# Performance work log

Measured on AMD Instinct MI355X. Metric: run time of the kernel, lower is better.

Reference implementation:

```python
import jax, jax.numpy as jnp
import numpy as np

B, L, D, H = 2, 1024, 1024, 16
HD = D // H
HIDDEN = 4 * D
EPS = 1e-6
SCALE = HD ** -0.5

# RoPE tables (head_dim is even, so rope_dim == head_dim)
_inv_freq = 1.0 / (10000.0 ** (np.arange(0, HD, 2, dtype=np.float32) / HD))
_freqs = np.arange(L, dtype=np.float32)[:, None] * _inv_freq[None, :]          # [L, HD/2]
COS = jnp.asarray(np.concatenate([np.cos(_freqs), np.cos(_freqs)], -1))        # [L, HD]
SIN = jnp.asarray(np.concatenate([np.sin(_freqs), np.sin(_freqs)], -1))
MASK = jnp.tril(jnp.ones((L, L), dtype=bool))                                   # causal


def _clin(xr, xi, Wr, Wi, br=None, bi=None):
    # complex linear: (a+bi)(c+di), weights stored [out, in] as in torch
    r = xr @ Wr.T - xi @ Wi.T
    i = xr @ Wi.T + xi @ Wr.T
    if br is not None:
        r = r + br
        i = i + bi
    return r, i


def _cln(xr, xi, gr, gi, br, bi):
    mr = xr.mean(-1, keepdims=True)
    mi = xi.mean(-1, keepdims=True)
    cr = xr - mr
    ci = xi - mi
    var = (cr * cr + ci * ci).mean(-1, keepdims=True)
    s = jnp.sqrt(var + EPS)
    nr = cr / s
    ni = ci / s
    return nr * gr - ni * gi + br, nr * gi + ni * gr + bi


def _rot_half(x):
    h = x.shape[-1] // 2
    return jnp.concatenate([-x[..., h:], x[..., :h]], -1)


def _rope(xr, xi):
    # apply same real rotation to real and imag parts (matches torch code)
    return (xr * COS + _rot_half(xr) * SIN, xi * COS + _rot_half(xi) * SIN)


def _split_heads(x):
    return x.reshape(B, L, H, HD).transpose(0, 2, 1, 3)  # [B,H,L,HD]


def _merge_heads(x):
    return x.transpose(0, 2, 1, 3).reshape(B, L, D)


def setup_inputs() -> dict:
    key = jax.random.key(0)
    ks = jax.random.split(key, 20)
    n = lambda k, shape, s=1.0: jax.random.normal(k, shape, dtype=jnp.float32) * s
    s_attn = (2.0 * (D + D)) ** -0.5
    s_fc1 = (2.0 * (D + HIDDEN)) ** -0.5
    s_fc2 = (2.0 * (HIDDEN + D)) ** -0.5
    return {
        'x_real': n(ks[0], (B, L, D)),
        'x_imag': n(ks[1], (B, L, D)),
        'Wq_r': n(ks[2], (D, D), s_attn), 'Wq_i': n(ks[3], (D, D), s_attn),
        'Wk_r': n(ks[4], (D, D), s_attn), 'Wk_i': n(ks[5], (D, D), s_attn),
        'Wv_r': n(ks[6], (D, D), s_attn), 'Wv_i': n(ks[7], (D, D), s_attn),
        'Wo_r': n(ks[8], (D, D), s_attn), 'Wo_i': n(ks[9], (D, D), s_attn),
        'bo_r': jnp.zeros((D,), jnp.float32), 'bo_i': jnp.zeros((D,), jnp.float32),
        'ln1_gr': jnp.ones((D,), jnp.float32), 'ln1_gi': jnp.zeros((D,), jnp.float32),
        'ln1_br': jnp.zeros((D,), jnp.float32), 'ln1_bi': jnp.zeros((D,), jnp.float32),
        'ln2_gr': jnp.ones((D,), jnp.float32), 'ln2_gi': jnp.zeros((D,), jnp.float32),
        'ln2_br': jnp.zeros((D,), jnp.float32), 'ln2_bi': jnp.zeros((D,), jnp.float32),
        'W1_r': n(ks[10], (HIDDEN, D), s_fc1), 'W1_i': n(ks[11], (HIDDEN, D), s_fc1),
        'b1_r': jnp.zeros((HIDDEN,), jnp.float32), 'b1_i': jnp.zeros((HIDDEN,), jnp.float32),
        'W2_r': n(ks[12], (D, HIDDEN), s_fc2), 'W2_i': n(ks[13], (D, HIDDEN), s_fc2),
        'b2_r': jnp.zeros((D,), jnp.float32), 'b2_i': jnp.zeros((D,), jnp.float32),
        'mod_b': n(ks[14], (HIDDEN,), 0.1),
    }


def reference(x_real, x_imag,
              Wq_r, Wq_i, Wk_r, Wk_i, Wv_r, Wv_i, Wo_r, Wo_i, bo_r, bo_i,
              ln1_gr, ln1_gi, ln1_br, ln1_bi, ln2_gr, ln2_gi, ln2_br, ln2_bi,
              W1_r, W1_i, b1_r, b1_i, W2_r, W2_i, b2_r, b2_i, mod_b):
    # --- attention sublayer (pre-LN) ---
    hr, hi = _cln(x_real, x_imag, ln1_gr, ln1_gi, ln1_br, ln1_bi)
    Qr, Qi = _clin(hr, hi, Wq_r, Wq_i)
    Kr, Ki = _clin(hr, hi, Wk_r, Wk_i)
    Vr, Vi = _clin(hr, hi, Wv_r, Wv_i)
    Qr, Qi, Kr, Ki = map(_split_heads, (Qr, Qi, Kr, Ki))
    Vr, Vi = _split_heads(Vr), _split_heads(Vi)
    Qr, Qi = _rope(Qr, Qi)
    Kr, Ki = _rope(Kr, Ki)
    # Hermitian inner product real part: Re(Q K*) = Qr.Kr + Qi.Ki
    scores = (jnp.einsum('bhld,bhmd->bhlm', Qr, Kr)
              + jnp.einsum('bhld,bhmd->bhlm', Qi, Ki)) * SCALE
    scores = jnp.where(MASK, scores, -jnp.inf)
    attn = jax.nn.softmax(scores, axis=-1)
    out_r = _merge_heads(jnp.einsum('bhlm,bhmd->bhld', attn, Vr))
    out_i = _merge_heads(jnp.einsum('bhlm,bhmd->bhld', attn, Vi))
    out_r, out_i = _clin(out_r, out_i, Wo_r, Wo_i, bo_r, bo_i)
    ar = x_real + out_r
    ai = x_imag + out_i
    # --- feed-forward sublayer (pre-LN) ---
    hr, hi = _cln(ar, ai, ln2_gr, ln2_gi, ln2_br, ln2_bi)
    fr, fi = _clin(hr, hi, W1_r, W1_i, b1_r, b1_i)
    # ModReLU: relu(|z| + b) * e^{i angle(z)}
    mag = jnp.sqrt(fr * fr + fi * fi)
    safe = jnp.where(mag > 0, mag, 1.0)
    act = jax.nn.relu(mag + mod_b)
    fr, fi = act * fr / safe, act * fi / safe
    fr, fi = _clin(fr, fi, W2_r, W2_i, b2_r, b2_i)
    return ar + fr, ai + fi
```

## Files before the change

### kernel.cpp

```cpp
#include <hip/hip_runtime.h>

#define Bq 2
#define Lq 1024
#define Dq 1024
#define Hq 16
#define HDq 64
#define HIDq 4096
#define Mq (Bq*Lq)

typedef __bf16 bf16x8 __attribute__((ext_vector_type(8)));
typedef float floatx4 __attribute__((ext_vector_type(4)));

__device__ __forceinline__ float us2f(unsigned short u){
  unsigned v = ((unsigned)u) << 16;
  return __builtin_bit_cast(float, v);
}
__device__ __forceinline__ unsigned short f2us(float f){
  unsigned u = __builtin_bit_cast(unsigned, f);
  u = u + 0x7fffu + ((u >> 16) & 1u);
  return (unsigned short)(u >> 16);
}

__global__ __launch_bounds__(256) void cvt4_kernel(
    const float* __restrict__ s0, const float* __restrict__ s1,
    const float* __restrict__ s2, const float* __restrict__ s3,
    unsigned short* __restrict__ d0, unsigned short* __restrict__ d1,
    unsigned short* __restrict__ d2, unsigned short* __restrict__ d3,
    int n)
{
  const int a = blockIdx.y;
  const float* s = (a==0) ? s0 : (a==1) ? s1 : (a==2) ? s2 : s3;
  unsigned short* d = (a==0) ? d0 : (a==1) ? d1 : (a==2) ? d2 : d3;
  const int i = (blockIdx.x * 256 + threadIdx.x) * 8;
  if (i >= n) return;
  float4 v0 = ((const float4*)(s + i))[0];
  float4 v1 = ((const float4*)(s + i))[1];
  ushort4 o0, o1;
  o0.x=f2us(v0.x); o0.y=f2us(v0.y); o0.z=f2us(v0.z); o0.w=f2us(v0.w);
  o1.x=f2us(v1.x); o1.y=f2us(v1.y); o1.z=f2us(v1.z); o1.w=f2us(v1.w);
  ((ushort4*)(d + i))[0] = o0;
  ((ushort4*)(d + i))[1] = o1;
}

__global__ __launch_bounds__(256) void cln_kernel(
    const float* __restrict__ xr, const float* __restrict__ xi,
    const float* __restrict__ gr, const float* __restrict__ gi,
    const float* __restrict__ br, const float* __restrict__ bi,
    unsigned short* __restrict__ outr, unsigned short* __restrict__ outi)
{
  const int row = blockIdx.x;
  const int t = threadIdx.x;
  const int lane = t & 63, wv = t >> 6;
  __shared__ float sred[8];

  float4 v4r = ((const float4*)(xr + (size_t)row*Dq))[t];
  float4 v4i = ((const float4*)(xi + (size_t)row*Dq))[t];
  float vr[4] = {v4r.x, v4r.y, v4r.z, v4r.w};
  float vi[4] = {v4i.x, v4i.y, v4i.z, v4i.w};
  float sr = vr[0]+vr[1]+vr[2]+vr[3];
  float si = vi[0]+vi[1]+vi[2]+vi[3];
  #pragma unroll
  for (int o=32;o>0;o>>=1){ sr += __shfl_down(sr,o,64); si += __shfl_down(si,o,64); }
  if (lane==0){ sred[wv]=sr; sred[4+wv]=si; }
  __syncthreads();
  float mr = (sred[0]+sred[1]+sred[2]+sred[3]) * (1.0f/Dq);
  float mi = (sred[4]+sred[5]+sred[6]+sred[7]) * (1.0f/Dq);
  float cr[4], ci[4], vs = 0.f;
  #pragma unroll
  for (int j=0;j<4;++j){ cr[j]=vr[j]-mr; ci[j]=vi[j]-mi; vs += cr[j]*cr[j]+ci[j]*ci[j]; }
  #pragma unroll
  for (int o=32;o>0;o>>=1) vs += __shfl_down(vs,o,64);
  __syncthreads();
  if (lane==0) sred[wv]=vs;
  __syncthreads();
  float var = (sred[0]+sred[1]+sred[2]+sred[3]) * (1.0f/Dq);
  float inv = rsqrtf(var + 1e-6f);

  float4 g4r = ((const float4*)gr)[t];
  float4 g4i = ((const float4*)gi)[t];
  float4 b4r = ((const float4*)br)[t];
  float4 b4i = ((const float4*)bi)[t];
  float grf[4] = {g4r.x,g4r.y,g4r.z,g4r.w};
  float gif[4] = {g4i.x,g4i.y,g4i.z,g4i.w};
  float brf[4] = {b4r.x,b4r.y,b4r.z,b4r.w};
  float bif[4] = {b4i.x,b4i.y,b4i.z,b4i.w};
  ushort4 o_r, o_i;
  unsigned short orr[4], oii[4];
  #pragma unroll
  for (int j=0;j<4;++j){
    float nr = cr[j]*inv, ni = ci[j]*inv;
    orr[j] = f2us(nr*grf[j] - ni*gif[j] + brf[j]);
    oii[j] = f2us(nr*gif[j] + ni*grf[j] + bif[j]);
  }
  o_r.x=orr[0]; o_r.y=orr[1]; o_r.z=orr[2]; o_r.w=orr[3];
  o_i.x=oii[0]; o_i.y=oii[1]; o_i.z=oii[2]; o_i.w=oii[3];
  ((ushort4*)(outr + (size_t)row*Dq))[t] = o_r;
  ((ushort4*)(outi + (size_t)row*Dq))[t] = o_i;
}

template<int EPI, bool ROPE>
__global__ __launch_bounds__(256,2) void cgemm_kernel(
    const unsigned short* __restrict__ Ar, const unsigned short* __restrict__ Ai,
    const unsigned short* __restrict__ Wr, const unsigned short* __restrict__ Wi,
    void* __restrict__ Cr, void* __restrict__ Ci,
    const float* __restrict__ biasR, const float* __restrict__ biasI,
    const float* __restrict__ resR, const float* __restrict__ resI,
    const float* __restrict__ modb,
    int Ndim, int Kdim)
{
  const int t = threadIdx.x;
  const int wv = t >> 6, lane = t & 63;
  const int quad = lane >> 4, l15 = lane & 15;
  const int m0 = blockIdx.x * 64, n0 = blockIdx.y * 64;

  __shared__ __align__(16) unsigned short sAr[64*40], sAi[64*40], sWr[64*40], sWi[64*40];

  floatx4 accRR[4], accII[4], accRI[4], accIR[4];
  floatx4 zero = {0.f,0.f,0.f,0.f};
  #pragma unroll
  for (int i=0;i<4;++i){ accRR[i]=zero; accII[i]=zero; accRI[i]=zero; accIR[i]=zero; }

  const int lr = t >> 2;
  const int lc = (t & 3) * 8;
  const unsigned short* pAr = Ar + (size_t)(m0+lr)*Kdim + lc;
  const unsigned short* pAi = Ai + (size_t)(m0+lr)*Kdim + lc;
  const unsigned short* pWr = Wr + (size_t)(n0+lr)*Kdim + lc;
  const unsigned short* pWi = Wi + (size_t)(n0+lr)*Kdim + lc;
  const int ldso = lr*40 + lc;
  const int arow = wv*16 + l15;

  const int nk = Kdim >> 5;
  for (int kk=0; kk<nk; ++kk){
    uint4 va = *(const uint4*)(pAr + kk*32);
    uint4 vb = *(const uint4*)(pAi + kk*32);
    uint4 vc = *(const uint4*)(pWr + kk*32);
    uint4 vd = *(const uint4*)(pWi + kk*32);
    __syncthreads();
    *(uint4*)&sAr[ldso] = va;
    *(uint4*)&sAi[ldso] = vb;
    *(uint4*)&sWr[ldso] = vc;
    *(uint4*)&sWi[ldso] = vd;
    __syncthreads();
    bf16x8 fAr = *(const bf16x8*)&sAr[arow*40 + quad*8];
    bf16x8 fAi = *(const bf16x8*)&sAi[arow*40 + quad*8];
    #pragma unroll
    for (int tt=0; tt<4; ++tt){
      const int brow = tt*16 + l15;
      bf16x8 fWr = *(const bf16x8*)&sWr[brow*40 + quad*8];
      bf16x8 fWi = *(const bf16x8*)&sWi[brow*40 + quad*8];
      accRR[tt] = __builtin_amdgcn_mfma_f32_16x16x32_bf16(fAr, fWr, accRR[tt], 0,0,0);
      accII[tt] = __builtin_amdgcn_mfma_f32_16x16x32_bf16(fAi, fWi, accII[tt], 0,0,0);
      accRI[tt] = __builtin_amdgcn_mfma_f32_16x16x32_bf16(fAr, fWi, accRI[tt], 0,0,0);
      accIR[tt] = __builtin_amdgcn_mfma_f32_16x16x32_bf16(fAi, fWr, accIR[tt], 0,0,0);
    }
  }

  float cr[4][4], ci[4][4];
  #pragma unroll
  for (int tt=0; tt<4; ++tt)
    #pragma unroll
    for (int r=0; r<4; ++r){
      cr[tt][r] = accRR[tt][r] - accII[tt][r];
      ci[tt][r] = accRI[tt][r] + accIR[tt][r];
    }

  if (ROPE){
    #pragma unroll
    for (int tt=0; tt<2; ++tt){
      const int j = tt*16 + l15;
      const float invf = powf(10000.0f, -(float)j * (1.0f/32.0f));
      #pragma unroll
      for (int r=0; r<4; ++r){
        const int gm = m0 + wv*16 + quad*4 + r;
        const int l = gm & (Lq-1);
        float s, c;
        sincosf((float)l * invf, &s, &c);
        float xr_ = cr[tt][r], yr_ = cr[tt+2][r];
        cr[tt][r]   = xr_*c - yr_*s;
        cr[tt+2][r] = yr_*c + xr_*s;
        float xi_ = ci[tt][r], yi_ = ci[tt+2][r];
        ci[tt][r]   = xi_*c - yi_*s;
        ci[tt+2][r] = yi_*c + xi_*s;
      }
    }
  }

  #pragma unroll
  for (int tt=0; tt<4; ++tt){
    const int gn = n0 + tt*16 + l15;
    float bR = 0.f, bI = 0.f, mb = 0.f;
    if (EPI >= 1){ bR = biasR[gn]; bI = biasI[gn]; }
    if (EPI == 2){ mb = modb[gn]; }
    #pragma unroll
    for (int r=0; r<4; ++r){
      const int gm = m0 + wv*16 + quad*4 + r;
      const size_t idx = (size_t)gm*Ndim + gn;
      float vr_ = cr[tt][r] + bR, vi_ = ci[tt][r] + bI;
      if (EPI == 1 || EPI == 3){ vr_ += resR[idx]; vi_ += resI[idx]; }
      if (EPI == 2){
        float mag = sqrtf(vr_*vr_ + vi_*vi_);
        float safe = (mag > 0.f) ? mag : 1.0f;
        float act = fmaxf(mag + mb, 0.f);
        float sc = act / safe;
        vr_ *= sc; vi_ *= sc;
      }
      if (EPI == 0 || EPI == 2){
        ((unsigned short*)Cr)[idx] = f2us(vr_);
        ((unsigned short*)Ci)[idx] = f2us(vi_);
      } else {
        ((float*)Cr)[idx] = vr_;
        ((float*)Ci)[idx] = vi_;
      }
    }
  }
}

__global__ __launch_bounds__(256) void vtrans_kernel(
    const unsigned short* __restrict__ Vr, const unsigned short* __restrict__ Vi,
    unsigned short* __restrict__ VTr, unsigned short* __restrict__ VTi)
{
  const int lt = blockIdx.x;
  const int bh = blockIdx.y;
  const int h = bh & (Hq-1), b = bh >> 4;
  const int t = threadIdx.x;
  __shared__ unsigned short sTr[64*65], sTi[64*65];

  const int row = t >> 2;
  const int dc  = (t & 3) * 16;
  const size_t g = ((size_t)(b*Lq) + lt*64 + row)*Dq + h*HDq + dc;
  uint4 a0 = *(const uint4*)(Vr + g);
  uint4 a1 = *(const uint4*)(Vr + g + 8);
  uint4 b0 = *(const uint4*)(Vi + g);
  uint4 b1 = *(const uint4*)(Vi + g + 8);
  const unsigned short* pa0 = (const unsigned short*)&a0;
  const unsigned short* pa1 = (const unsigned short*)&a1;
  const unsigned short* pb0 = (const unsigned short*)&b0;
  const unsigned short* pb1 = (const unsigned short*)&b1;
  #pragma unroll
  for (int e=0;e<8;++e){
    sTr[(dc+e)*65 + row]   = pa0[e];
    sTr[(dc+8+e)*65 + row] = pa1[e];
    sTi[(dc+e)*65 + row]   = pb0[e];
    sTi[(dc+8+e)*65 + row] = pb1[e];
  }
  __syncthreads();
  const int d  = t >> 2;
  const int lc = (t & 3) * 16;
  unsigned short bufr[16], bufi[16];
  #pragma unroll
  for (int e=0;e<16;++e){
    bufr[e] = sTr[d*65 + lc + e];
    bufi[e] = sTi[d*65 + lc + e];
  }
  const size_t og = ((size_t)bh*HDq + d)*Lq + lt*64 + lc;
  *(uint4*)(VTr + og)     = *(const uint4*)&bufr[0];
  *(uint4*)(VTr + og + 8) = *(const uint4*)&bufr[8];
  *(uint4*)(VTi + og)     = *(const uint4*)&bufi[0];
  *(uint4*)(VTi + og + 8) = *(const uint4*)&bufi[8];
}

__device__ __forceinline__ int swz(int v){ return v ^ ((v >> 4) & 7); }

__global__ __launch_bounds__(256,2) void fattn_kernel(
    const unsigned short* __restrict__ Qr, const unsigned short* __restrict__ Qi,
    const unsigned short* __restrict__ Kr, const unsigned short* __restrict__ Ki,
    const unsigned short* __restrict__ VTr, const unsigned short* __restrict__ VTi,
    unsigned short* __restrict__ Or, unsigned short* __restrict__ Oi)
{
  const int qt = (int)(gridDim.x - 1 - blockIdx.x);
  const int bh = blockIdx.y;
  const int h = bh & (Hq-1), b = bh >> 4;
  const int t = threadIdx.x;
  const int w = t >> 6, lane = t & 63;
  const int quad = lane >> 4, l15 = lane & 15;

  __shared__ __align__(16) unsigned short sKr[4096], sKi[4096], sVr[4096], sVi[4096];
  __shared__ __align__(16) unsigned short sP[64*72];

  const size_t qbase = ((size_t)(b*Lq) + qt*64 + w*16 + l15)*Dq + h*HDq;
  bf16x8 qr_lo = *(const bf16x8*)(Qr + qbase + quad*8);
  bf16x8 qr_hi = *(const bf16x8*)(Qr + qbase + 32 + quad*8);
  bf16x8 qi_lo = *(const bf16x8*)(Qi + qbase + quad*8);
  bf16x8 qi_hi = *(const bf16x8*)(Qi + qbase + 32 + quad*8);

  const floatx4 fzero = {0.f,0.f,0.f,0.f};
  floatx4 aOr[4], aOi[4];
  #pragma unroll
  for (int i=0;i<4;++i){ aOr[i]=fzero; aOi[i]=fzero; }
  float m_run[4] = {-1e30f,-1e30f,-1e30f,-1e30f};
  float l_run[4] = {0.f,0.f,0.f,0.f};

  const int srow = t >> 2;
  const int sns  = srow >> 4;
  const int sl15 = srow & 15;
  const int q8   = (t & 3) * 2;
  const int dstA = sns*1024 + swz(q8*16 + sl15)*8;
  const int dstB = sns*1024 + swz((q8+1)*16 + sl15)*8;

  const int rd0 = swz(quad*16 + l15)*8;
  const int rd1 = swz((4+quad)*16 + l15)*8;

  for (int kt = 0; kt <= qt; ++kt){
    const size_t kg = ((size_t)(b*Lq) + kt*64 + srow)*Dq + h*HDq + q8*8;
    uint4 ka = *(const uint4*)(Kr + kg);
    uint4 kb = *(const uint4*)(Kr + kg + 8);
    uint4 kc = *(const uint4*)(Ki + kg);
    uint4 kd = *(const uint4*)(Ki + kg + 8);
    const size_t vg = ((size_t)bh*HDq + srow)*Lq + kt*64 + q8*8;
    uint4 va = *(const uint4*)(VTr + vg);
    uint4 vb = *(const uint4*)(VTr + vg + 8);
    uint4 vc = *(const uint4*)(VTi + vg);
    uint4 vd = *(const uint4*)(VTi + vg + 8);
    __syncthreads();
    *(uint4*)&sKr[dstA] = ka;  *(uint4*)&sKr[dstB] = kb;
    *(uint4*)&sKi[dstA] = kc;  *(uint4*)&sKi[dstB] = kd;
    *(uint4*)&sVr[dstA] = va;  *(uint4*)&sVr[dstB] = vb;
    *(uint4*)&sVi[dstA] = vc;  *(uint4*)&sVi[dstB] = vd;
    __syncthreads();

    floatx4 sc[4];
    #pragma unroll
    for (int ns=0; ns<4; ++ns){
      floatx4 x = fzero;
      x = __builtin_amdgcn_mfma_f32_16x16x32_bf16(qr_lo, *(const bf16x8*)&sKr[ns*1024 + rd0], x, 0,0,0);
      x = __builtin_amdgcn_mfma_f32_16x16x32_bf16(qr_hi, *(const bf16x8*)&sKr[ns*1024 + rd1], x, 0,0,0);
      x = __builtin_amdgcn_mfma_f32_16x16x32_bf16(qi_lo, *(const bf16x8*)&sKi[ns*1024 + rd0], x, 0,0,0);
      x = __builtin_amdgcn_mfma_f32_16x16x32_bf16(qi_hi, *(const bf16x8*)&sKi[ns*1024 + rd1], x, 0,0,0);
      sc[ns] = x;
    }

    const bool diag = (kt == qt);
    float rmax[4] = {-1e30f,-1e30f,-1e30f,-1e30f};
    #pragma unroll
    for (int ns=0; ns<4; ++ns){
      #pragma unroll
      for (int r=0; r<4; ++r){
        float s = sc[ns][r] * 0.125f;
        if (diag && (ns*16 + l15 > w*16 + quad*4 + r)) s = -1e30f;
        sc[ns][r] = s;
        rmax[r] = fmaxf(rmax[r], s);
      }
    }
    #pragma unroll
    for (int off=1; off<16; off<<=1){
      #pragma unroll
      for (int r=0; r<4; ++r) rmax[r] = fmaxf(rmax[r], __shfl_xor(rmax[r], off, 64));
    }

    float alpha[4], rsum[4];
    #pragma unroll
    for (int r=0; r<4; ++r){
      float mn = fmaxf(m_run[r], rmax[r]);
      alpha[r] = __expf(m_run[r] - mn);
      m_run[r] = mn;
      rsum[r] = 0.f;
    }
    #pragma unroll
    for (int ns=0; ns<4; ++ns){
      #pragma unroll
      for (int r=0; r<4; ++r){
        float p = __expf(sc[ns][r] - m_run[r]);
        rsum[r] += p;
        sP[(w*16 + quad*4 + r)*72 + ns*16 + l15] = f2us(p);
      }
    }
    #pragma unroll
    for (int off=1; off<16; off<<=1){
      #pragma unroll
      for (int r=0; r<4; ++r) rsum[r] += __shfl_xor(rsum[r], off, 64);
    }
    #pragma unroll
    for (int r=0; r<4; ++r) l_run[r] = l_run[r]*alpha[r] + rsum[r];
    #pragma unroll
    for (int ds=0; ds<4; ++ds)
      #pragma unroll
      for (int r=0; r<4; ++r){ aOr[ds][r] *= alpha[r]; aOi[ds][r] *= alpha[r]; }

    #pragma unroll
    for (int step=0; step<2; ++step){
      bf16x8 pf = *(const bf16x8*)&sP[(w*16 + l15)*72 + step*32 + quad*8];
      const int ro = (step==0) ? rd0 : rd1;
      #pragma unroll
      for (int ds=0; ds<4; ++ds){
        aOr[ds] = __builtin_amdgcn_mfma_f32_16x16x32_bf16(pf, *(const bf16x8*)&sVr[ds*1024 + ro], aOr[ds], 0,0,0);
        aOi[ds] = __builtin_amdgcn_mfma_f32_16x16x32_bf16(pf, *(const bf16x8*)&sVi[ds*1024 + ro], aOi[ds], 0,0,0);
      }
    }
  }

  #pragma unroll
  for (int r=0; r<4; ++r){
    const float il = 1.0f / l_run[r];
    const size_t ob = ((size_t)(b*Lq) + qt*64 + w*16 + quad*4 + r)*Dq + h*HDq;
    #pragma unroll
    for (int ds=0; ds<4; ++ds){
      Or[ob + ds*16 + l15] = f2us(aOr[ds][r] * il);
      Oi[ob + ds*16 + l15] = f2us(aOi[ds][r] * il);
    }
  }
}

extern "C" void kernel_launch(void* const* d_in, const int* in_sizes, int n_in,
                              void* d_out, int out_size, void* d_ws, size_t ws_size,
                              hipStream_t stream)
{
  const float* x_r    = (const float*)d_in[0];
  const float* x_i    = (const float*)d_in[1];
  const float* Wq_r   = (const float*)d_in[2];
  const float* Wq_i   = (const float*)d_in[3];
  const float* Wk_r   = (const float*)d_in[4];
  const float* Wk_i   = (const float*)d_in[5];
  const float* Wv_r   = (const float*)d_in[6];
  const float* Wv_i   = (const float*)d_in[7];
  const float* Wo_r   = (const float*)d_in[8];
  const float* Wo_i   = (const float*)d_in[9];
  const float* bo_r   = (const float*)d_in[10];
  const float* bo_i   = (const float*)d_in[11];
  const float* ln1_gr = (const float*)d_in[12];
  const float* ln1_gi = (const float*)d_in[13];
  const float* ln1_br = (const float*)d_in[14];
  const float* ln1_bi = (const float*)d_in[15];
  const float* ln2_gr = (const float*)d_in[16];
  const float* ln2_gi = (const float*)d_in[17];
  const float* ln2_br = (const float*)d_in[18];
  const float* ln2_bi = (const float*)d_in[19];
  const float* W1_r   = (const float*)d_in[20];
  const float* W1_i   = (const float*)d_in[21];
  const float* b1_r   = (const float*)d_in[22];
  const float* b1_i   = (const float*)d_in[23];
  const float* W2_r   = (const float*)d_in[24];
  const float* W2_i   = (const float*)d_in[25];
  const float* b2_r   = (const float*)d_in[26];
  const float* b2_i   = (const float*)d_in[27];
  const float* mod_b  = (const float*)d_in[28];

  char* wsb = (char*)d_ws;
  const size_t MB = 1024*1024;
  unsigned short* bWq_r = (unsigned short*)(wsb + 0*MB);
  unsigned short* bWq_i = (unsigned short*)(wsb + 2*MB);
  unsigned short* bWk_r = (unsigned short*)(wsb + 4*MB);
  unsigned short* bWk_i = (unsigned short*)(wsb + 6*MB);
  unsigned short* bWv_r = (unsigned short*)(wsb + 8*MB);
  unsigned short* bWv_i = (unsigned short*)(wsb + 10*MB);
  unsigned short* bWo_r = (unsigned short*)(wsb + 12*MB);
  unsigned short* bWo_i = (unsigned short*)(wsb + 14*MB);
  unsigned short* bW1_r = (unsigned short*)(wsb + 16*MB);
  unsigned short* bW1_i = (unsigned short*)(wsb + 24*MB);
  unsigned short* bW2_r = (unsigned short*)(wsb + 32*MB);
  unsigned short* bW2_i = (unsigned short*)(wsb + 40*MB);
  unsigned short* hr  = (unsigned short*)(wsb + 48*MB);
  unsigned short* hi_ = (unsigned short*)(wsb + 52*MB);
  unsigned short* Qr  = (unsigned short*)(wsb + 56*MB);
  unsigned short* Qi  = (unsigned short*)(wsb + 60*MB);
  unsigned short* Kr  = (unsigned short*)(wsb + 64*MB);
  unsigned short* Ki  = (unsigned short*)(wsb + 68*MB);
  unsigned short* Vr  = (unsigned short*)(wsb + 72*MB);
  unsigned short* Vi  = (unsigned short*)(wsb + 76*MB);
  unsigned short* VTr = (unsigned short*)(wsb + 80*MB);
  unsigned short* VTi = (unsigned short*)(wsb + 84*MB);
  unsigned short* Or  = hr;
  unsigned short* Oi  = hi_;
  unsigned short* h2r = Qr;
  unsigned short* h2i = Qi;
  unsigned short* fr  = (unsigned short*)(wsb + 64*MB);
  unsigned short* fi  = (unsigned short*)(wsb + 80*MB);

  float* outR = (float*)d_out;
  float* outI = outR + (size_t)Mq*Dq;

  const dim3 blk(256);
  const dim3 gD(Mq/64, Dq/64);
  const dim3 gH(Mq/64, HIDq/64);

  const int nDD = Dq*Dq;
  const int nDH = Dq*HIDq;
  cvt4_kernel<<<dim3(nDD/2048, 4), blk, 0, stream>>>(Wq_r, Wq_i, Wk_r, Wk_i,
      bWq_r, bWq_i, bWk_r, bWk_i, nDD);
  cvt4_kernel<<<dim3(nDD/2048, 4), blk, 0, stream>>>(Wv_r, Wv_i, Wo_r, Wo_i,
      bWv_r, bWv_i, bWo_r, bWo_i, nDD);
  cvt4_kernel<<<dim3(nDH/2048, 4), blk, 0, stream>>>(W1_r, W1_i, W2_r, W2_i,
      bW1_r, bW1_i, bW2_r, bW2_i, nDH);

  cln_kernel<<<Mq, blk, 0, stream>>>(x_r, x_i, ln1_gr, ln1_gi, ln1_br, ln1_bi, hr, hi_);
  cgemm_kernel<0,true ><<<gD, blk, 0, stream>>>(hr, hi_, bWq_r, bWq_i, Qr, Qi,
      nullptr, nullptr, nullptr, nullptr, nullptr, Dq, Dq);
  cgemm_kernel<0,true ><<<gD, blk, 0, stream>>>(hr, hi_, bWk_r, bWk_i, Kr, Ki,
      nullptr, nullptr, nullptr, nullptr, nullptr, Dq, Dq);
  cgemm_kernel<0,false><<<gD, blk, 0, stream>>>(hr, hi_, bWv_r, bWv_i, Vr, Vi,
      nullptr, nullptr, nullptr, nullptr, nullptr, Dq, Dq);
  vtrans_kernel<<<dim3(16, 32), blk, 0, stream>>>(Vr, Vi, VTr, VTi);
  fattn_kernel<<<dim3(16, 32), blk, 0, stream>>>(Qr, Qi, Kr, Ki, VTr, VTi, Or, Oi);
  cgemm_kernel<1,false><<<gD, blk, 0, stream>>>(Or, Oi, bWo_r, bWo_i, outR, outI,
      bo_r, bo_i, x_r, x_i, nullptr, Dq, Dq);
  cln_kernel<<<Mq, blk, 0, stream>>>(outR, outI, ln2_gr, ln2_gi, ln2_br, ln2_bi, h2r, h2i);
  cgemm_kernel<2,false><<<gH, blk, 0, stream>>>(h2r, h2i, bW1_r, bW1_i, fr, fi,
      b1_r, b1_i, nullptr, nullptr, mod_b, HIDq, Dq);
  cgemm_kernel<3,false><<<gD, blk, 0, stream>>>(fr, fi, bW2_r, bW2_i, outR, outI,
      b2_r, b2_i, outR, outI, nullptr, Dq, HIDq);
}
```

Before: 550.6 us.

## Rewrite complex GEMM with 32x32 MFMA, direct global-to-LDS loads, fused QKV

Replaces the 16x16x32 MFMA complex GEMM with a 128-thread kernel that uses 32x32x16 MFMAs and a 64-wide K step. Tiles are loaded straight into XOR-swizzled shared memory with global_load_lds, skipping the register staging step and reducing bank conflicts. The Q, K and V weights are converted into one contiguous buffer, so a single launch computes all three projections and applies RoPE only to the Q/K column blocks. This aims for better MFMA efficiency, fewer launches and more reuse of the A tile. In exchange there are fewer waves per block and more accumulator registers per thread, and loads still have no double buffering.

```diff
diff --git a/kernel.cpp b/kernel.cpp
--- a/kernel.cpp
+++ b/kernel.cpp
@@ -10,15 +10,18 @@
 
 typedef __bf16 bf16x8 __attribute__((ext_vector_type(8)));
 typedef float floatx4 __attribute__((ext_vector_type(4)));
-
-__device__ __forceinline__ float us2f(unsigned short u){
-  unsigned v = ((unsigned)u) << 16;
-  return __builtin_bit_cast(float, v);
-}
+typedef float floatx16 __attribute__((ext_vector_type(16)));
+
 __device__ __forceinline__ unsigned short f2us(float f){
   unsigned u = __builtin_bit_cast(unsigned, f);
   u = u + 0x7fffu + ((u >> 16) & 1u);
   return (unsigned short)(u >> 16);
+}
+
+__device__ __forceinline__ void gld16(const unsigned short* g, unsigned short* l){
+  __builtin_amdgcn_global_load_lds(
+      (const __attribute__((address_space(1))) unsigned int*)g,
+      (__attribute__((address_space(3))) unsigned int*)l, 16, 0, 0);
 }
 
 __global__ __launch_bounds__(256) void cvt4_kernel(
@@ -98,104 +101,133 @@
   ((ushort4*)(outi + (size_t)row*Dq))[t] = o_i;
 }
 
-template<int EPI, bool ROPE>
-__global__ __launch_bounds__(256,2) void cgemm_kernel(
+template<int EPI, bool ROPE, bool SPLIT3>
+__global__ __launch_bounds__(128,2) void cgemm32_kernel(
     const unsigned short* __restrict__ Ar, const unsigned short* __restrict__ Ai,
     const unsigned short* __restrict__ Wr, const unsigned short* __restrict__ Wi,
-    void* __restrict__ Cr, void* __restrict__ Ci,
+    void* __restrict__ Cr0, void* __restrict__ Ci0,
+    void* __restrict__ Cr1, void* __restrict__ Ci1,
+    void* __restrict__ Cr2, void* __restrict__ Ci2,
     const float* __restrict__ biasR, const float* __restrict__ biasI,
     const float* __restrict__ resR, const float* __restrict__ resI,
     const float* __restrict__ modb,
     int Ndim, int Kdim)
 {
   const int t = threadIdx.x;
-  const int wv = t >> 6, lane = t & 63;
-  const int quad = lane >> 4, l15 = lane & 15;
+  const int w = t >> 6, l = t & 63;
+  const int l31 = l & 31, lhi = l >> 5;
   const int m0 = blockIdx.x * 64, n0 = blockIdx.y * 64;
 
-  __shared__ __align__(16) unsigned short sAr[64*40], sAi[64*40], sWr[64*40], sWi[64*40];
-
-  floatx4 accRR[4], accII[4], accRI[4], accIR[4];
-  floatx4 zero = {0.f,0.f,0.f,0.f};
-  #pragma unroll
-  for (int i=0;i<4;++i){ accRR[i]=zero; accII[i]=zero; accRI[i]=zero; accIR[i]=zero; }
-
-  const int lr = t >> 2;
-  const int lc = (t & 3) * 8;
-  const unsigned short* pAr = Ar + (size_t)(m0+lr)*Kdim + lc;
-  const unsigned short* pAi = Ai + (size_t)(m0+lr)*Kdim + lc;
-  const unsigned short* pWr = Wr + (size_t)(n0+lr)*Kdim + lc;
-  const unsigned short* pWi = Wi + (size_t)(n0+lr)*Kdim + lc;
-  const int ldso = lr*40 + lc;
-  const int arow = wv*16 + l15;
-
-  const int nk = Kdim >> 5;
+  __shared__ __align__(16) unsigned short sAr[64*64], sAi[64*64], sWr[64*64], sWi[64*64];
+
+  floatx16 accRR[2], accII[2], accRI[2], accIR[2];
+  #pragma unroll
+  for (int i=0;i<2;++i){
+    #pragma unroll
+    for (int r=0;r<16;++r){ accRR[i][r]=0.f; accII[i][r]=0.f; accRI[i][r]=0.f; accIR[i][r]=0.f; }
+  }
+
+  const int srow = t >> 3;
+  const int lc = (((t & 7) ^ ((t >> 3) & 7))) * 8;
+  const unsigned short* pAr = Ar + (size_t)(m0 + srow)*Kdim + lc;
+  const unsigned short* pAi = Ai + (size_t)(m0 + srow)*Kdim + lc;
+  const unsigned short* pWr = Wr + (size_t)(n0 + srow)*Kdim + lc;
+  const unsigned short* pWi = Wi + (size_t)(n0 + srow)*Kdim + lc;
+  const int dst0 = t * 8;
+
+  const int arow = w*32 + l31;
+  int aoff[4], woff0[4], woff1[4];
+  #pragma unroll
+  for (int kh=0; kh<4; ++kh){
+    const int c = kh*2 + lhi;
+    aoff[kh]  = arow*64      + ((c ^ (arow & 7)) * 8);
+    woff0[kh] = l31*64       + ((c ^ (l31 & 7)) * 8);
+    woff1[kh] = (32+l31)*64  + ((c ^ (l31 & 7)) * 8);
+  }
+
+  const int nk = Kdim >> 6;
   for (int kk=0; kk<nk; ++kk){
-    uint4 va = *(const uint4*)(pAr + kk*32);
-    uint4 vb = *(const uint4*)(pAi + kk*32);
-    uint4 vc = *(const uint4*)(pWr + kk*32);
-    uint4 vd = *(const uint4*)(pWi + kk*32);
+    #pragma unroll
+    for (int j=0;j<4;++j){
+      const size_t so = (size_t)j * 16 * Kdim;
+      gld16(pAr + so, &sAr[dst0 + j*1024]);
+      gld16(pAi + so, &sAi[dst0 + j*1024]);
+      gld16(pWr + so, &sWr[dst0 + j*1024]);
+      gld16(pWi + so, &sWi[dst0 + j*1024]);
+    }
+    pAr += 64; pAi += 64; pWr += 64; pWi += 64;
     __syncthreads();
-    *(uint4*)&sAr[ldso] = va;
-    *(uint4*)&sAi[ldso] = vb;
-    *(uint4*)&sWr[ldso] = vc;
-    *(uint4*)&sWi[ldso] = vd;
+    #pragma unroll
+    for (int kh=0; kh<4; ++kh){
+      bf16x8 fAr  = *(const bf16x8*)&sAr[aoff[kh]];
+      bf16x8 fAi  = *(const bf16x8*)&sAi[aoff[kh]];
+      bf16x8 fW0r = *(const bf16x8*)&sWr[woff0[kh]];
+      bf16x8 fW0i = *(const bf16x8*)&sWi[woff0[kh]];
+      bf16x8 fW1r = *(const bf16x8*)&sWr[woff1[kh]];
+      bf16x8 fW1i = *(const bf16x8*)&sWi[woff1[kh]];
+      accRR[0] = __builtin_amdgcn_mfma_f32_32x32x16_bf16(fAr, fW0r, accRR[0], 0,0,0);
+      accII[0] = __builtin_amdgcn_mfma_f32_32x32x16_bf16(fAi, fW0i, accII[0], 0,0,0);
+      accRI[0] = __builtin_amdgcn_mfma_f32_32x32x16_bf16(fAr, fW0i, accRI[0], 0,0,0);
+      accIR[0] = __builtin_amdgcn_mfma_f32_32x32x16_bf16(fAi, fW0r, accIR[0], 0,0,0);
+      accRR[1] = __builtin_amdgcn_mfma_f32_32x32x16_bf16(fAr, fW1r, accRR[1], 0,0,0);
+      accII[1] = __builtin_amdgcn_mfma_f32_32x32x16_bf16(fAi, fW1i, accII[1], 0,0,0);
+      accRI[1] = __builtin_amdgcn_mfma_f32_32x32x16_bf16(fAr, fW1i, accRI[1], 0,0,0);
+      accIR[1] = __builtin_amdgcn_mfma_f32_32x32x16_bf16(fAi, fW1r, accIR[1], 0,0,0);
+    }
     __syncthreads();
-    bf16x8 fAr = *(const bf16x8*)&sAr[arow*40 + quad*8];
-    bf16x8 fAi = *(const bf16x8*)&sAi[arow*40 + quad*8];
-    #pragma unroll
-    for (int tt=0; tt<4; ++tt){
-      const int brow = tt*16 + l15;
-      bf16x8 fWr = *(const bf16x8*)&sWr[brow*40 + quad*8];
-      bf16x8 fWi = *(const bf16x8*)&sWi[brow*40 + quad*8];
-      accRR[tt] = __builtin_amdgcn_mfma_f32_16x16x32_bf16(fAr, fWr, accRR[tt], 0,0,0);
-      accII[tt] = __builtin_amdgcn_mfma_f32_16x16x32_bf16(fAi, fWi, accII[tt], 0,0,0);
-      accRI[tt] = __builtin_amdgcn_mfma_f32_16x16x32_bf16(fAr, fWi, accRI[tt], 0,0,0);
-      accIR[tt] = __builtin_amdgcn_mfma_f32_16x16x32_bf16(fAi, fWr, accIR[tt], 0,0,0);
-    }
-  }
-
-  float cr[4][4], ci[4][4];
-  #pragma unroll
-  for (int tt=0; tt<4; ++tt)
-    #pragma unroll
-    for (int r=0; r<4; ++r){
-      cr[tt][r] = accRR[tt][r] - accII[tt][r];
-      ci[tt][r] = accRI[tt][r] + accIR[tt][r];
-    }
-
-  if (ROPE){
-    #pragma unroll
-    for (int tt=0; tt<2; ++tt){
-      const int j = tt*16 + l15;
-      const float invf = powf(10000.0f, -(float)j * (1.0f/32.0f));
-      #pragma unroll
-      for (int r=0; r<4; ++r){
-        const int gm = m0 + wv*16 + quad*4 + r;
-        const int l = gm & (Lq-1);
-        float s, c;
-        sincosf((float)l * invf, &s, &c);
-        float xr_ = cr[tt][r], yr_ = cr[tt+2][r];
-        cr[tt][r]   = xr_*c - yr_*s;
-        cr[tt+2][r] = yr_*c + xr_*s;
-        float xi_ = ci[tt][r], yi_ = ci[tt+2][r];
-        ci[tt][r]   = xi_*c - yi_*s;
-        ci[tt+2][r] = yi_*c + xi_*s;
-      }
-    }
-  }
-
-  #pragma unroll
-  for (int tt=0; tt<4; ++tt){
-    const int gn = n0 + tt*16 + l15;
+  }
+
+  float cr[2][16], ci[2][16];
+  #pragma unroll
+  for (int nf=0; nf<2; ++nf)
+    #pragma unroll
+    for (int r=0;r<16;++r){
+      cr[nf][r] = accRR[nf][r] - accII[nf][r];
+      ci[nf][r] = accRI[nf][r] + accIR[nf][r];
+    }
+
+  const bool doRope = ROPE && (!SPLIT3 || (n0 < 2048));
+  if (doRope){
+    const float invf = powf(10000.0f, -(float)l31 * (1.0f/32.0f));
+    #pragma unroll
+    for (int r=0;r<16;++r){
+      const int gm = m0 + w*32 + (r&3) + 8*(r>>2) + 4*lhi;
+      float s, c;
+      sincosf((float)(gm & (Lq-1)) * invf, &s, &c);
+      float xr_ = cr[0][r], yr_ = cr[1][r];
+      cr[0][r] = xr_*c - yr_*s;  cr[1][r] = yr_*c + xr_*s;
+      float xi_ = ci[0][r], yi_ = ci[1][r];
+      ci[0][r] = xi_*c - yi_*s;  ci[1][r] = yi_*c + xi_*s;
+    }
+  }
+
+  unsigned short *oR16 = nullptr, *oI16 = nullptr;
+  float *oR32 = nullptr, *oI32 = nullptr;
+  int ncol0, Nst;
+  if (SPLIT3){
+    const int aid = n0 >> 10;
+    void* vr = (aid==0) ? Cr0 : ((aid==1) ? Cr1 : Cr2);
+    void* vi = (aid==0) ? Ci0 : ((aid==1) ? Ci1 : Ci2);
+    oR16 = (unsigned short*)vr; oI16 = (unsigned short*)vi;
+    ncol0 = n0 & 1023; Nst = 1024;
+  } else {
+    oR16 = (unsigned short*)Cr0; oI16 = (unsigned short*)Ci0;
+    oR32 = (float*)Cr0;          oI32 = (float*)Ci0;
+    ncol0 = n0; Nst = Ndim;
+  }
+
+  #pragma unroll
+  for (int nf=0; nf<2; ++nf){
+    const int gn = n0 + nf*32 + l31;
+    const int cn = ncol0 + nf*32 + l31;
     float bR = 0.f, bI = 0.f, mb = 0.f;
     if (EPI >= 1){ bR = biasR[gn]; bI = biasI[gn]; }
     if (EPI == 2){ mb = modb[gn]; }
     #pragma unroll
-    for (int r=0; r<4; ++r){
-      const int gm = m0 + wv*16 + quad*4 + r;
-      const size_t idx = (size_t)gm*Ndim + gn;
-      float vr_ = cr[tt][r] + bR, vi_ = ci[tt][r] + bI;
+    for (int r=0;r<16;++r){
+      const int gm = m0 + w*32 + (r&3) + 8*(r>>2) + 4*lhi;
+      const size_t idx = (size_t)gm*Nst + cn;
+      float vr_ = cr[nf][r] + bR, vi_ = ci[nf][r] + bI;
       if (EPI == 1 || EPI == 3){ vr_ += resR[idx]; vi_ += resI[idx]; }
       if (EPI == 2){
         float mag = sqrtf(vr_*vr_ + vi_*vi_);
@@ -205,11 +237,11 @@
         vr_ *= sc; vi_ *= sc;
       }
       if (EPI == 0 || EPI == 2){
-        ((unsigned short*)Cr)[idx] = f2us(vr_);
-        ((unsigned short*)Ci)[idx] = f2us(vi_);
+        oR16[idx] = f2us(vr_);
+        oI16[idx] = f2us(vi_);
       } else {
-        ((float*)Cr)[idx] = vr_;
-        ((float*)Ci)[idx] = vi_;
+        oR32[idx] = vr_;
+        oI32[idx] = vi_;
       }
     }
   }
@@ -245,14 +277,14 @@
   }
   __syncthreads();
   const int d  = t >> 2;
-  const int lc = (t & 3) * 16;
+  const int lcx = (t & 3) * 16;
   unsigned short bufr[16], bufi[16];
   #pragma unroll
   for (int e=0;e<16;++e){
-    bufr[e] = sTr[d*65 + lc + e];
-    bufi[e] = sTi[d*65 + lc + e];
-  }
-  const size_t og = ((size_t)bh*HDq + d)*Lq + lt*64 + lc;
+    bufr[e] = sTr[d*65 + lcx + e];
+    bufi[e] = sTi[d*65 + lcx + e];
+  }
+  const size_t og = ((size_t)bh*HDq + d)*Lq + lt*64 + lcx;
   *(uint4*)(VTr + og)     = *(const uint4*)&bufr[0];
   *(uint4*)(VTr + og + 8) = *(const uint4*)&bufr[8];
   *(uint4*)(VTi + og)     = *(const uint4*)&bufi[0];
@@ -436,12 +468,8 @@
 
   char* wsb = (char*)d_ws;
   const size_t MB = 1024*1024;
-  unsigned short* bWq_r = (unsigned short*)(wsb + 0*MB);
-  unsigned short* bWq_i = (unsigned short*)(wsb + 2*MB);
-  unsigned short* bWk_r = (unsigned short*)(wsb + 4*MB);
-  unsigned short* bWk_i = (unsigned short*)(wsb + 6*MB);
-  unsigned short* bWv_r = (unsigned short*)(wsb + 8*MB);
-  unsigned short* bWv_i = (unsigned short*)(wsb + 10*MB);
+  unsigned short* bQKV_r = (unsigned short*)(wsb + 0*MB);
+  unsigned short* bQKV_i = (unsigned short*)(wsb + 6*MB);
   unsigned short* bWo_r = (unsigned short*)(wsb + 12*MB);
   unsigned short* bWo_i = (unsigned short*)(wsb + 14*MB);
   unsigned short* bW1_r = (unsigned short*)(wsb + 16*MB);
@@ -469,32 +497,32 @@
   float* outI = outR + (size_t)Mq*Dq;
 
   const dim3 blk(256);
-  const dim3 gD(Mq/64, Dq/64);
-  const dim3 gH(Mq/64, HIDq/64);
+  const dim3 blk128(128);
 
   const int nDD = Dq*Dq;
   const int nDH = Dq*HIDq;
-  cvt4_kernel<<<dim3(nDD/2048, 4), blk, 0, stream>>>(Wq_r, Wq_i, Wk_r, Wk_i,
-      bWq_r, bWq_i, bWk_r, bWk_i, nDD);
-  cvt4_kernel<<<dim3(nDD/2048, 4), blk, 0, stream>>>(Wv_r, Wv_i, Wo_r, Wo_i,
-      bWv_r, bWv_i, bWo_r, bWo_i, nDD);
+  cvt4_kernel<<<dim3(nDD/2048, 4), blk, 0, stream>>>(Wq_r, Wk_r, Wv_r, Wo_r,
+      bQKV_r, bQKV_r + (size_t)nDD, bQKV_r + (size_t)2*nDD, bWo_r, nDD);
+  cvt4_kernel<<<dim3(nDD/2048, 4), blk, 0, stream>>>(Wq_i, Wk_i, Wv_i, Wo_i,
+      bQKV_i, bQKV_i + (size_t)nDD, bQKV_i + (size_t)2*nDD, bWo_i, nDD);
   cvt4_kernel<<<dim3(nDH/2048, 4), blk, 0, stream>>>(W1_r, W1_i, W2_r, W2_i,
       bW1_r, bW1_i, bW2_r, bW2_i, nDH);
 
   cln_kernel<<<Mq, blk, 0, stream>>>(x_r, x_i, ln1_gr, ln1_gi, ln1_br, ln1_bi, hr, hi_);
-  cgemm_kernel<0,true ><<<gD, blk, 0, stream>>>(hr, hi_, bWq_r, bWq_i, Qr, Qi,
-      nullptr, nullptr, nullptr, nullptr, nullptr, Dq, Dq);
-  cgemm_kernel<0,true ><<<gD, blk, 0, stream>>>(hr, hi_, bWk_r, bWk_i, Kr, Ki,
-      nullptr, nullptr, nullptr, nullptr, nullptr, Dq, Dq);
-  cgemm_kernel<0,false><<<gD, blk, 0, stream>>>(hr, hi_, bWv_r, bWv_i, Vr, Vi,
-      nullptr, nullptr, nullptr, nullptr, nullptr, Dq, Dq);
+  cgemm32_kernel<0,true,true><<<dim3(Mq/64, 3072/64), blk128, 0, stream>>>(
+      hr, hi_, bQKV_r, bQKV_i,
+      Qr, Qi, Kr, Ki, Vr, Vi,
+      nullptr, nullptr, nullptr, nullptr, nullptr, 3072, Dq);
   vtrans_kernel<<<dim3(16, 32), blk, 0, stream>>>(Vr, Vi, VTr, VTi);
   fattn_kernel<<<dim3(16, 32), blk, 0, stream>>>(Qr, Qi, Kr, Ki, VTr, VTi, Or, Oi);
-  cgemm_kernel<1,false><<<gD, blk, 0, stream>>>(Or, Oi, bWo_r, bWo_i, outR, outI,
+  cgemm32_kernel<1,false,false><<<dim3(Mq/64, Dq/64), blk128, 0, stream>>>(
+      Or, Oi, bWo_r, bWo_i, outR, outI, nullptr, nullptr, nullptr, nullptr,
       bo_r, bo_i, x_r, x_i, nullptr, Dq, Dq);
   cln_kernel<<<Mq, blk, 0, stream>>>(outR, outI, ln2_gr, ln2_gi, ln2_br, ln2_bi, h2r, h2i);
-  cgemm_kernel<2,false><<<gH, blk, 0, stream>>>(h2r, h2i, bW1_r, bW1_i, fr, fi,
+  cgemm32_kernel<2,false,false><<<dim3(Mq/64, HIDq/64), blk128, 0, stream>>>(
+      h2r, h2i, bW1_r, bW1_i, fr, fi, nullptr, nullptr, nullptr, nullptr,
       b1_r, b1_i, nullptr, nullptr, mod_b, HIDq, Dq);
-  cgemm_kernel<3,false><<<gD, blk, 0, stream>>>(fr, fi, bW2_r, bW2_i, outR, outI,
+  cgemm32_kernel<3,false,false><<<dim3(Mq/64, Dq/64), blk128, 0, stream>>>(
+      fr, fi, bW2_r, bW2_i, outR, outI, nullptr, nullptr, nullptr, nullptr,
       b2_r, b2_i, outR, outI, nullptr, Dq, HIDq);
 }
```

New measurement: 550.8 us. About the same (+0.0%).
